# Kernel optimization log

Hardware: AMD Instinct MI355X
Metric: run time of the kernel (lower is better)

The kernel has to match this reference:

```python
import jax, jax.numpy as jnp
import numpy as np
from jax import lax

B, C, W, H = 32, 64, 32, 32
HEADS, RED = 4, 16
D = C // HEADS


def setup_inputs() -> dict:
    key = jax.random.key(0)
    ks = jax.random.split(key, 16)
    s = 0.05
    return {
        "x": jax.random.normal(ks[0], (B, C, W, H), jnp.float32),
        "Wq": jax.random.normal(ks[1], (C, C), jnp.float32) * s,
        "bq": jnp.zeros((C,), jnp.float32),
        "Wk": jax.random.normal(ks[2], (C, C), jnp.float32) * s,
        "bk": jnp.zeros((C,), jnp.float32),
        "Wv": jax.random.normal(ks[3], (C, C), jnp.float32) * s,
        "bv": jnp.zeros((C,), jnp.float32),
        "rel_h": jax.random.normal(ks[4], (1, HEADS, D, 1, H), jnp.float32),
        "rel_w": jax.random.normal(ks[5], (1, HEADS, D, W, 1), jnp.float32),
        "ln_g": jnp.ones((C, W, H), jnp.float32),
        "ln_b": jnp.zeros((C, W, H), jnp.float32),
        "ca_w1": jax.random.normal(ks[6], (C // RED, C), jnp.float32) * s,
        "ca_b1": jnp.zeros((C // RED,), jnp.float32),
        "ca_w2": jax.random.normal(ks[7], (C, C // RED), jnp.float32) * s,
        "ca_b2": jnp.zeros((C,), jnp.float32),
        "sa_w": jax.random.normal(ks[8], (1, 2, 7, 7), jnp.float32) * s,
        "sa_b": jnp.zeros((1,), jnp.float32),
    }


def reference(x, Wq, bq, Wk, bk, Wv, bv, rel_h, rel_w, ln_g, ln_b,
              ca_w1, ca_b1, ca_w2, ca_b2, sa_w, sa_b):
    b, c, w, h = x.shape
    n = w * h
    d = c // HEADS

    def conv1x1(t, wt, bt):
        return jnp.einsum('bchw,oc->bohw', t, wt) + bt[None, :, None, None]

    # ---- MHSA branch ----
    q = conv1x1(x, Wq, bq).reshape(b, HEADS, d, n)
    k = conv1x1(x, Wk, bk).reshape(b, HEADS, d, n)
    v = conv1x1(x, Wv, bv).reshape(b, HEADS, d, n)
    cc = jnp.einsum('bhdi,bhdj->bhij', q, k)                  # content-content
    pos = (rel_h + rel_w).reshape(1, HEADS, d, n)              # [1,H,d,N]
    cp = jnp.einsum('zhdi,bhdj->bhij', pos, q)                 # content-position
    att = jax.nn.softmax(cc + cp, axis=-1)                     # [b,H,N,N]
    out = jnp.einsum('bhdj,bhij->bhdi', v, att).reshape(b, c, w, h)
    # LayerNorm over (C,W,H)
    mu = jnp.mean(out, axis=(1, 2, 3), keepdims=True)
    var = jnp.var(out, axis=(1, 2, 3), keepdims=True)
    ln = (out - mu) * lax.rsqrt(var + 1e-5) * ln_g[None] + ln_b[None]
    mhsa = ln + x

    # ---- CBAM branch ----
    avg = jnp.mean(x, axis=(2, 3))                             # [b,c]
    mx = jnp.max(x, axis=(2, 3))

    def mlp(f):
        hid = jax.nn.relu(jnp.einsum('bc,oc->bo', f, ca_w1) + ca_b1)
        return jnp.einsum('bc,oc->bo', hid, ca_w2) + ca_b2

    ch_att = jax.nn.sigmoid(mlp(avg) + mlp(mx))[:, :, None, None]
    xc = ch_att * x
    feat = jnp.stack([jnp.mean(xc, axis=1), jnp.max(xc, axis=1)], axis=1)  # [b,2,w,h]
    sp = lax.conv_general_dilated(feat, sa_w, (1, 1), 'SAME',
                                  dimension_numbers=('NCHW', 'OIHW', 'NCHW'))
    sp = sp + sa_b[None, :, None, None]
    cbam = jax.nn.sigmoid(sp) * xc

    return mhsa + cbam + x
```

## Files before the change

### kernel.cpp

```cpp
#include <hip/hip_runtime.h>

#define BB 32
#define CC 64
#define WW 32
#define HHT 32
#define NH 4
#define DHD 16
#define NN 1024
#define LOG2E 1.4426950408889634f

typedef __attribute__((ext_vector_type(8))) short bf16x8;
typedef __attribute__((ext_vector_type(4))) float f32x4;

__device__ __forceinline__ float wave_sum(float v) {
#pragma unroll
  for (int off = 32; off > 0; off >>= 1) v += __shfl_down(v, off, 64);
  return v;
}
__device__ __forceinline__ float wave_max(float v) {
#pragma unroll
  for (int off = 32; off > 0; off >>= 1) v = fmaxf(v, __shfl_down(v, off, 64));
  return v;
}
__device__ __forceinline__ unsigned bf16pair(float lo, float hi) {
  unsigned a = __float_as_uint(lo), b = __float_as_uint(hi);
  a += 0x7FFFu + ((a >> 16) & 1u);
  b += 0x7FFFu + ((b >> 16) & 1u);
  return (a >> 16) | (b & 0xFFFF0000u);
}
__device__ __forceinline__ short bf16s(float f) {
  unsigned a = __float_as_uint(f);
  a += 0x7FFFu + ((a >> 16) & 1u);
  return (short)(a >> 16);
}

__global__ __launch_bounds__(256) void qkv_kernel(
    const float* __restrict__ x,
    const float* __restrict__ Wq, const float* __restrict__ bq,
    const float* __restrict__ Wk, const float* __restrict__ bk,
    const float* __restrict__ Wv, const float* __restrict__ bv,
    short* __restrict__ KQ, short* __restrict__ Vb, float* __restrict__ lnzero)
{
  __shared__ __align__(16) short Ws[192 * 72];
  const int tid = threadIdx.x;
  const int b = blockIdx.y, nt = blockIdx.x;

  if (tid < 192) {
    const int m = tid >> 4, dd = tid & 15;
    const int mat = m >> 2, h = m & 3;
    const float* src = (mat == 0 ? Wk : (mat == 1 ? Wq : Wv)) + (h * 16 + dd) * CC;
    const float scale = (mat == 0) ? LOG2E : 1.f;
    short* dst = Ws + tid * 72;
#pragma unroll
    for (int c8 = 0; c8 < 8; ++c8) {
      const float4 f0 = *reinterpret_cast<const float4*>(src + c8 * 8);
      const float4 f1 = *reinterpret_cast<const float4*>(src + c8 * 8 + 4);
      uint4 u;
      u.x = bf16pair(f0.x*scale, f0.y*scale); u.y = bf16pair(f0.z*scale, f0.w*scale);
      u.z = bf16pair(f1.x*scale, f1.y*scale); u.w = bf16pair(f1.z*scale, f1.w*scale);
      *reinterpret_cast<uint4*>(dst + c8 * 8) = u;
    }
  }
  if (blockIdx.x == 0 && blockIdx.y == 0 && tid < 64) lnzero[tid] = 0.f;
  __syncthreads();

  const int wid = tid >> 6, lane = tid & 63, Q = lane >> 4, il = lane & 15;
  const int n = nt * 64 + wid * 16 + il;
  const float* xb = x + (size_t)b * CC * NN;

  union { bf16x8 s; unsigned u[4]; } bfr[2];
#pragma unroll
  for (int half = 0; half < 2; ++half) {
#pragma unroll
    for (int p = 0; p < 4; ++p) {
      const int c0 = 32 * half + 8 * Q + 2 * p;
      const float f0 = xb[(size_t)c0 * NN + n];
      const float f1 = xb[(size_t)(c0 + 1) * NN + n];
      bfr[half].u[p] = bf16pair(f0, f1);
    }
  }

  const f32x4 zero4 = {0.f, 0.f, 0.f, 0.f};
  f32x4 acc[12];
#pragma unroll
  for (int m = 0; m < 12; ++m) {
    const short* wr = Ws + (m * 16 + il) * 72;
    const bf16x8 a0 = *reinterpret_cast<const bf16x8*>(wr + 8 * Q);
    const bf16x8 a1 = *reinterpret_cast<const bf16x8*>(wr + 32 + 8 * Q);
    acc[m] = __builtin_amdgcn_mfma_f32_16x16x32_bf16(a0, bfr[0].s, zero4, 0, 0, 0);
    acc[m] = __builtin_amdgcn_mfma_f32_16x16x32_bf16(a1, bfr[1].s, acc[m], 0, 0, 0);
  }

#pragma unroll
  for (int m = 0; m < 12; ++m) {
    const int mat = m >> 2, h = m & 3;
    const float bsc = (mat == 0) ? LOG2E : 1.f;
    const float4 bias = *reinterpret_cast<const float4*>(
        (mat == 0 ? bk : (mat == 1 ? bq : bv)) + h * 16 + 4 * Q);
    const float v0 = acc[m][0] + bias.x*bsc, v1 = acc[m][1] + bias.y*bsc;
    const float v2 = acc[m][2] + bias.z*bsc, v3 = acc[m][3] + bias.w*bsc;
    if (mat < 2) {
      uint2 pk;
      pk.x = bf16pair(v0, v1); pk.y = bf16pair(v2, v3);
      *reinterpret_cast<uint2*>(KQ + ((size_t)(b * NH + h) * NN + n) * 32 +
                                (mat == 0 ? 0 : 16) + 4 * Q) = pk;
    } else {
      short* vb = Vb + ((size_t)(b * NH + h) * 16 + 4 * Q) * NN + n;
      vb[0]            = bf16s(v0);
      vb[(size_t)NN]   = bf16s(v1);
      vb[2*(size_t)NN] = bf16s(v2);
      vb[3*(size_t)NN] = bf16s(v3);
    }
  }
}

__global__ __launch_bounds__(256) void flash_kernel(
    const short* __restrict__ KQ, const short* __restrict__ Vb,
    const float* __restrict__ rel_h, const float* __restrict__ rel_w,
    float* __restrict__ attnout, float* __restrict__ lnsum, float* __restrict__ lnsum2)
{
  const int tid = threadIdx.x;
  const int wid = tid >> 6, lane = tid & 63;
  const int Q = lane >> 4, il = lane & 15;
  const int bh = blockIdx.x;
  const int h = bh & 3, b = bh >> 2;
  const int ibase = blockIdx.y * 256 + wid * 64;

  bf16x8 bfrag[4];
#pragma unroll
  for (int g2 = 0; g2 < 4; ++g2) {
    const int i = ibase + g2*16 + il;
    if (Q < 2) {
      bfrag[g2] = *reinterpret_cast<const bf16x8*>(KQ + ((size_t)bh*NN + i)*32 + 16 + 8*Q);
    } else {
      const int wrow = i >> 5, hcol = i & 31;
      union { bf16x8 s; unsigned u[4]; } t;
#pragma unroll
      for (int p = 0; p < 4; ++p) {
        const int d0 = 8*(Q-2) + 2*p;
        const float f0 = LOG2E*(rel_h[(h*DHD + d0)*HHT + hcol] + rel_w[(h*DHD + d0)*WW + wrow]);
        const float f1 = LOG2E*(rel_h[(h*DHD + d0+1)*HHT + hcol] + rel_w[(h*DHD + d0+1)*WW + wrow]);
        t.u[p] = bf16pair(f0, f1);
      }
      bfrag[g2] = t.s;
    }
  }

  const short* KQb = KQ + (size_t)bh*NN*32;
  const short* Vbb = Vb + ((size_t)bh*16 + il)*NN;
  const f32x4 zero4 = {0.f, 0.f, 0.f, 0.f};
  f32x4 acc[4] = {zero4, zero4, zero4, zero4};
  float lp[4] = {0.f, 0.f, 0.f, 0.f};

  bf16x8 agc[4]; uint2 vloc[2], vhic[2];
#pragma unroll
  for (int g = 0; g < 4; ++g)
    agc[g] = *reinterpret_cast<const bf16x8*>(KQb + (size_t)(16*g + il)*32 + 8*Q);
#pragma unroll
  for (int hh = 0; hh < 2; ++hh) {
    const short* vp = Vbb + 32*hh + 4*Q;
    vloc[hh] = *reinterpret_cast<const uint2*>(vp);
    vhic[hh] = *reinterpret_cast<const uint2*>(vp + 16);
  }

  for (int jt = 0; jt < NN; jt += 64) {
    const int jn = (jt + 64) & (NN - 1);
    bf16x8 agn[4]; uint2 vlon[2], vhin[2];
#pragma unroll
    for (int g = 0; g < 4; ++g)
      agn[g] = *reinterpret_cast<const bf16x8*>(KQb + (size_t)(jn + 16*g + il)*32 + 8*Q);
#pragma unroll
    for (int hh = 0; hh < 2; ++hh) {
      const short* vp = Vbb + jn + 32*hh + 4*Q;
      vlon[hh] = *reinterpret_cast<const uint2*>(vp);
      vhin[hh] = *reinterpret_cast<const uint2*>(vp + 16);
    }

    union { bf16x8 s; unsigned u[4]; } bv0, bv1;
    bv0.u[0] = vloc[0].x; bv0.u[1] = vloc[0].y; bv0.u[2] = vhic[0].x; bv0.u[3] = vhic[0].y;
    bv1.u[0] = vloc[1].x; bv1.u[1] = vloc[1].y; bv1.u[2] = vhic[1].x; bv1.u[3] = vhic[1].y;

#pragma unroll
    for (int g2 = 0; g2 < 4; ++g2) {
      float p[4][4];
      unsigned pk[4][2];
#pragma unroll
      for (int g = 0; g < 4; ++g) {
        const f32x4 s = __builtin_amdgcn_mfma_f32_16x16x32_bf16(agc[g], bfrag[g2], zero4, 0, 0, 0);
#pragma unroll
        for (int r = 0; r < 4; ++r) { p[g][r] = __builtin_amdgcn_exp2f(s[r]); lp[g2] += p[g][r]; }
        pk[g][0] = bf16pair(p[g][0], p[g][1]);
        pk[g][1] = bf16pair(p[g][2], p[g][3]);
      }
#pragma unroll
      for (int hh = 0; hh < 2; ++hh) {
        union { bf16x8 s; unsigned u[4]; } ap;
        ap.u[0] = pk[2*hh][0];   ap.u[1] = pk[2*hh][1];
        ap.u[2] = pk[2*hh+1][0]; ap.u[3] = pk[2*hh+1][1];
        acc[g2] = __builtin_amdgcn_mfma_f32_16x16x32_bf16(ap.s, hh ? bv1.s : bv0.s, acc[g2], 0, 0, 0);
      }
    }
#pragma unroll
    for (int g = 0; g < 4; ++g) agc[g] = agn[g];
#pragma unroll
    for (int hh = 0; hh < 2; ++hh) { vloc[hh] = vlon[hh]; vhic[hh] = vhin[hh]; }
  }

  float s1 = 0.f, s2 = 0.f;
#pragma unroll
  for (int g2 = 0; g2 < 4; ++g2) {
    float l = lp[g2];
    l += __shfl_xor(l, 16, 64);
    l += __shfl_xor(l, 32, 64);
#pragma unroll
    for (int r = 0; r < 4; ++r) {
      const float li = __shfl(l, 4*Q + r, 64);
      const float v = acc[g2][r] / li;
      const int ig = ibase + g2*16 + 4*Q + r;
      attnout[((size_t)b*CC + h*DHD + il)*NN + ig] = v;
      s1 += v; s2 += v*v;
    }
  }
  s1 = wave_sum(s1); s2 = wave_sum(s2);
  __shared__ float r1[4], r2[4];
  if (lane == 0) { r1[wid] = s1; r2[wid] = s2; }
  __syncthreads();
  if (tid == 0) {
    atomicAdd(&lnsum[b],  r1[0]+r1[1]+r1[2]+r1[3]);
    atomicAdd(&lnsum2[b], r2[0]+r2[1]+r2[2]+r2[3]);
  }
}

__global__ __launch_bounds__(256) void cbamstats_kernel(
    const float* __restrict__ x, float* __restrict__ avg, float* __restrict__ mx)
{
  const int bc = blockIdx.x, tid = threadIdx.x;
  const float* p = x + (size_t)bc*NN;
  float s = 0.f, m = -3.0e38f;
  for (int u = tid; u < NN; u += 256) { const float v = p[u]; s += v; m = fmaxf(m, v); }
  s = wave_sum(s); m = wave_max(m);
  __shared__ float rs[4], rm[4];
  const int wid = tid >> 6, lane = tid & 63;
  if (lane == 0) { rs[wid] = s; rm[wid] = m; }
  __syncthreads();
  if (tid == 0) {
    avg[bc] = (rs[0]+rs[1]+rs[2]+rs[3]) * (1.f/NN);
    mx[bc]  = fmaxf(fmaxf(rm[0], rm[1]), fmaxf(rm[2], rm[3]));
  }
}

__global__ __launch_bounds__(256) void mlpfeat_kernel(
    const float* __restrict__ x, const float* __restrict__ avg, const float* __restrict__ mxv,
    const float* __restrict__ w1, const float* __restrict__ b1,
    const float* __restrict__ w2, const float* __restrict__ b2,
    float* __restrict__ chv, float* __restrict__ feat)
{
  const int b = blockIdx.y, qq = blockIdx.x, tid = threadIdx.x;
  __shared__ float sa[CC], sm[CC], sch[CC];
  __shared__ float ps[4][64], pm[4][64];
  if (tid < CC) { sa[tid] = avg[b*CC + tid]; sm[tid] = mxv[b*CC + tid]; }
  __syncthreads();
  if (tid < CC) {
    float s = 2.f * b2[tid];
#pragma unroll
    for (int o = 0; o < 4; ++o) {
      float ha = b1[o], hm = b1[o];
#pragma unroll
      for (int k = 0; k < CC; ++k) { ha += w1[o*CC + k]*sa[k]; hm += w1[o*CC + k]*sm[k]; }
      s += w2[tid*4 + o] * (fmaxf(ha, 0.f) + fmaxf(hm, 0.f));
    }
    const float c = 1.f/(1.f + __expf(-s));
    sch[tid] = c;
    if (qq == 0) chv[b*CC + tid] = c;
  }
  __syncthreads();
  const int nl = tid & 63, cg = tid >> 6;
  const int n = qq*64 + nl;
  float s = 0.f, m = -3.0e38f;
#pragma unroll
  for (int c = cg*16; c < cg*16 + 16; ++c) {
    const float v = sch[c] * x[((size_t)b*CC + c)*NN + n];
    s += v; m = fmaxf(m, v);
  }
  ps[cg][nl] = s; pm[cg][nl] = m;
  __syncthreads();
  if (cg == 0) {
    const float S = ps[0][nl]+ps[1][nl]+ps[2][nl]+ps[3][nl];
    const float M = fmaxf(fmaxf(pm[0][nl], pm[1][nl]), fmaxf(pm[2][nl], pm[3][nl]));
    feat[(size_t)b*2*NN + n]      = S * (1.f/CC);
    feat[(size_t)b*2*NN + NN + n] = M;
  }
}

__global__ __launch_bounds__(256) void final_kernel(
    const float* __restrict__ x, const float* __restrict__ attn,
    const float* __restrict__ ln_g, const float* __restrict__ ln_b,
    const float* __restrict__ feat, const float* __restrict__ ch,
    const float* __restrict__ lnsum, const float* __restrict__ lnsum2,
    const float* __restrict__ sa_w, const float* __restrict__ sa_b,
    float* __restrict__ out)
{
  const int b = blockIdx.y;
  const int c0 = blockIdx.z * 16;
  const int n = blockIdx.x*256 + threadIdx.x;
  const int w = n >> 5, hh = n & 31;
  __shared__ float sch[CC];
  __shared__ float swt[98];
  if (threadIdx.x < CC) sch[threadIdx.x] = ch[b*CC + threadIdx.x];
  if (threadIdx.x < 98) swt[threadIdx.x] = sa_w[threadIdx.x];
  __syncthreads();

  float s = sa_b[0];
#pragma unroll
  for (int ci = 0; ci < 2; ++ci)
#pragma unroll
    for (int kh = 0; kh < 7; ++kh) {
      const int wy = w + kh - 3;
      if (wy < 0 || wy >= WW) continue;
#pragma unroll
      for (int kw = 0; kw < 7; ++kw) {
        const int hx = hh + kw - 3;
        if (hx < 0 || hx >= HHT) continue;
        s += feat[((size_t)(b*2) + ci)*NN + wy*HHT + hx] * swt[ci*49 + kh*7 + kw];
      }
    }
  const float sg = 1.f/(1.f + __expf(-s));
  const float inv = 1.f/(CC*NN);
  const float m = lnsum[b]*inv;
  const float var = lnsum2[b]*inv - m*m;
  const float r = rsqrtf(var + 1e-5f);
#pragma unroll
  for (int c = c0; c < c0 + 16; ++c) {
    const size_t idx = ((size_t)b*CC + c)*NN + n;
    const float xa = x[idx];
    const float ln = (attn[idx] - m) * r * ln_g[c*NN + n] + ln_b[c*NN + n];
    out[idx] = ln + 2.f*xa + sg * sch[c] * xa;
  }
}

extern "C" void kernel_launch(void* const* d_in, const int* in_sizes, int n_in,
                              void* d_out, int out_size, void* d_ws, size_t ws_size,
                              hipStream_t stream)
{
  const float* x     = (const float*)d_in[0];
  const float* Wq    = (const float*)d_in[1];
  const float* bq    = (const float*)d_in[2];
  const float* Wk    = (const float*)d_in[3];
  const float* bk    = (const float*)d_in[4];
  const float* Wv    = (const float*)d_in[5];
  const float* bv    = (const float*)d_in[6];
  const float* rel_h = (const float*)d_in[7];
  const float* rel_w = (const float*)d_in[8];
  const float* ln_g  = (const float*)d_in[9];
  const float* ln_b  = (const float*)d_in[10];
  const float* cw1   = (const float*)d_in[11];
  const float* cb1   = (const float*)d_in[12];
  const float* cw2   = (const float*)d_in[13];
  const float* cb2   = (const float*)d_in[14];
  const float* saw   = (const float*)d_in[15];
  const float* sab   = (const float*)d_in[16];
  float* out = (float*)d_out;

  short* KQ = (short*)d_ws;
  short* Vb = KQ + (size_t)128*1024*32;
  float* fs = (float*)(Vb + (size_t)128*16*1024);
  float* lnsum  = fs;
  float* lnsum2 = fs + 32;
  float* avg    = fs + 64;
  float* mxv    = avg + 2048;
  float* chv    = mxv + 2048;
  float* feat   = chv + 2048;
  float* attn   = out;

  qkv_kernel<<<dim3(16, BB), 256, 0, stream>>>(x, Wq, bq, Wk, bk, Wv, bv, KQ, Vb, lnsum);
  flash_kernel<<<dim3(BB*NH, 4), 256, 0, stream>>>(KQ, Vb, rel_h, rel_w, attn, lnsum, lnsum2);
  cbamstats_kernel<<<BB*CC, 256, 0, stream>>>(x, avg, mxv);
  mlpfeat_kernel<<<dim3(16, BB), 256, 0, stream>>>(x, avg, mxv, cw1, cb1, cw2, cb2, chv, feat);
  final_kernel<<<dim3(4, BB, 4), 256, 0, stream>>>(x, attn, ln_g, ln_b, feat, chv, lnsum, lnsum2, saw, sab, out);
}
```

Measured before the change: 167.2 us.

## Precompute bf16 weights once, stage KQ stores via LDS, double flash grid

A new one-block prep kernel converts the QKV weights and biases to bf16 (log2e-scaled for K) in global memory once, instead of every qkv block converting them into shared memory. The qkv kernel loops per head and stages K/Q tiles through LDS so that global KQ writes are coalesced. The flash kernel gives each wave 32 query rows instead of 64 and launches twice as many blocks (1024), which raises occupancy and spreads work over more CUs. The cost is that each block streams the full K/V sequence for half as many queries, doubling total K/V reads, and the extra prep launch adds overhead.

```diff
diff --git a/kernel.cpp b/kernel.cpp
--- a/kernel.cpp
+++ b/kernel.cpp
@@ -34,83 +34,94 @@
   return (short)(a >> 16);
 }
 
-__global__ __launch_bounds__(256) void qkv_kernel(
-    const float* __restrict__ x,
+__global__ __launch_bounds__(256) void prep_kernel(
     const float* __restrict__ Wq, const float* __restrict__ bq,
     const float* __restrict__ Wk, const float* __restrict__ bk,
     const float* __restrict__ Wv, const float* __restrict__ bv,
-    short* __restrict__ KQ, short* __restrict__ Vb, float* __restrict__ lnzero)
-{
-  __shared__ __align__(16) short Ws[192 * 72];
+    short* __restrict__ Wb, float* __restrict__ bb, float* __restrict__ lnzero)
+{
   const int tid = threadIdx.x;
-  const int b = blockIdx.y, nt = blockIdx.x;
-
+  for (int idx = tid; idx < 192*32; idx += 256) {
+    const int row = idx >> 5, p = idx & 31;
+    const int m = row >> 4, dd = row & 15, mat = m >> 2, h = m & 3;
+    const float* src = (mat == 0 ? Wk : (mat == 1 ? Wq : Wv)) + (h*16 + dd)*CC + 2*p;
+    const float sc = (mat == 0) ? LOG2E : 1.f;
+    reinterpret_cast<unsigned*>(Wb)[row*32 + p] = bf16pair(src[0]*sc, src[1]*sc);
+  }
   if (tid < 192) {
-    const int m = tid >> 4, dd = tid & 15;
-    const int mat = m >> 2, h = m & 3;
-    const float* src = (mat == 0 ? Wk : (mat == 1 ? Wq : Wv)) + (h * 16 + dd) * CC;
-    const float scale = (mat == 0) ? LOG2E : 1.f;
-    short* dst = Ws + tid * 72;
-#pragma unroll
-    for (int c8 = 0; c8 < 8; ++c8) {
-      const float4 f0 = *reinterpret_cast<const float4*>(src + c8 * 8);
-      const float4 f1 = *reinterpret_cast<const float4*>(src + c8 * 8 + 4);
-      uint4 u;
-      u.x = bf16pair(f0.x*scale, f0.y*scale); u.y = bf16pair(f0.z*scale, f0.w*scale);
-      u.z = bf16pair(f1.x*scale, f1.y*scale); u.w = bf16pair(f1.z*scale, f1.w*scale);
-      *reinterpret_cast<uint4*>(dst + c8 * 8) = u;
-    }
-  }
-  if (blockIdx.x == 0 && blockIdx.y == 0 && tid < 64) lnzero[tid] = 0.f;
-  __syncthreads();
-
+    const int m = tid >> 4, dd = tid & 15, mat = m >> 2, h = m & 3;
+    const float* bs = (mat == 0 ? bk : (mat == 1 ? bq : bv));
+    bb[tid] = bs[h*16 + dd] * ((mat == 0) ? LOG2E : 1.f);
+  }
+  if (tid < 64) lnzero[tid] = 0.f;
+}
+
+__global__ __launch_bounds__(256) void qkv_kernel(
+    const float* __restrict__ x, const short* __restrict__ Wb,
+    const float* __restrict__ bb, short* __restrict__ KQ, short* __restrict__ Vb)
+{
+  __shared__ short KQt[4*16*36];
+  const int tid = threadIdx.x;
   const int wid = tid >> 6, lane = tid & 63, Q = lane >> 4, il = lane & 15;
-  const int n = nt * 64 + wid * 16 + il;
+  const int b = blockIdx.y;
+  const int nbase = blockIdx.x*64 + wid*16;
+  const int n = nbase + il;
   const float* xb = x + (size_t)b * CC * NN;
+  short* tw = KQt + wid*576;
 
   union { bf16x8 s; unsigned u[4]; } bfr[2];
 #pragma unroll
   for (int half = 0; half < 2; ++half) {
 #pragma unroll
     for (int p = 0; p < 4; ++p) {
-      const int c0 = 32 * half + 8 * Q + 2 * p;
-      const float f0 = xb[(size_t)c0 * NN + n];
-      const float f1 = xb[(size_t)(c0 + 1) * NN + n];
+      const int c0 = 32*half + 8*Q + 2*p;
+      const float f0 = xb[(size_t)c0*NN + n];
+      const float f1 = xb[(size_t)(c0+1)*NN + n];
       bfr[half].u[p] = bf16pair(f0, f1);
     }
   }
 
   const f32x4 zero4 = {0.f, 0.f, 0.f, 0.f};
-  f32x4 acc[12];
-#pragma unroll
-  for (int m = 0; m < 12; ++m) {
-    const short* wr = Ws + (m * 16 + il) * 72;
-    const bf16x8 a0 = *reinterpret_cast<const bf16x8*>(wr + 8 * Q);
-    const bf16x8 a1 = *reinterpret_cast<const bf16x8*>(wr + 32 + 8 * Q);
-    acc[m] = __builtin_amdgcn_mfma_f32_16x16x32_bf16(a0, bfr[0].s, zero4, 0, 0, 0);
-    acc[m] = __builtin_amdgcn_mfma_f32_16x16x32_bf16(a1, bfr[1].s, acc[m], 0, 0, 0);
-  }
-
-#pragma unroll
-  for (int m = 0; m < 12; ++m) {
-    const int mat = m >> 2, h = m & 3;
-    const float bsc = (mat == 0) ? LOG2E : 1.f;
-    const float4 bias = *reinterpret_cast<const float4*>(
-        (mat == 0 ? bk : (mat == 1 ? bq : bv)) + h * 16 + 4 * Q);
-    const float v0 = acc[m][0] + bias.x*bsc, v1 = acc[m][1] + bias.y*bsc;
-    const float v2 = acc[m][2] + bias.z*bsc, v3 = acc[m][3] + bias.w*bsc;
-    if (mat < 2) {
-      uint2 pk;
-      pk.x = bf16pair(v0, v1); pk.y = bf16pair(v2, v3);
-      *reinterpret_cast<uint2*>(KQ + ((size_t)(b * NH + h) * NN + n) * 32 +
-                                (mat == 0 ? 0 : 16) + 4 * Q) = pk;
-    } else {
-      short* vb = Vb + ((size_t)(b * NH + h) * 16 + 4 * Q) * NN + n;
-      vb[0]            = bf16s(v0);
-      vb[(size_t)NN]   = bf16s(v1);
-      vb[2*(size_t)NN] = bf16s(v2);
-      vb[3*(size_t)NN] = bf16s(v3);
-    }
+#pragma unroll
+  for (int h = 0; h < NH; ++h) {
+    const short* wk_ = Wb + ((h     )*16 + il)*64;
+    const short* wq_ = Wb + ((4 + h)*16 + il)*64;
+    const short* wv_ = Wb + ((8 + h)*16 + il)*64;
+    f32x4 ak = __builtin_amdgcn_mfma_f32_16x16x32_bf16(
+        *reinterpret_cast<const bf16x8*>(wk_ + 8*Q), bfr[0].s, zero4, 0, 0, 0);
+    ak = __builtin_amdgcn_mfma_f32_16x16x32_bf16(
+        *reinterpret_cast<const bf16x8*>(wk_ + 32 + 8*Q), bfr[1].s, ak, 0, 0, 0);
+    f32x4 aq = __builtin_amdgcn_mfma_f32_16x16x32_bf16(
+        *reinterpret_cast<const bf16x8*>(wq_ + 8*Q), bfr[0].s, zero4, 0, 0, 0);
+    aq = __builtin_amdgcn_mfma_f32_16x16x32_bf16(
+        *reinterpret_cast<const bf16x8*>(wq_ + 32 + 8*Q), bfr[1].s, aq, 0, 0, 0);
+    f32x4 av = __builtin_amdgcn_mfma_f32_16x16x32_bf16(
+        *reinterpret_cast<const bf16x8*>(wv_ + 8*Q), bfr[0].s, zero4, 0, 0, 0);
+    av = __builtin_amdgcn_mfma_f32_16x16x32_bf16(
+        *reinterpret_cast<const bf16x8*>(wv_ + 32 + 8*Q), bfr[1].s, av, 0, 0, 0);
+
+    const float4 bk4 = *reinterpret_cast<const float4*>(bb + (h     )*16 + 4*Q);
+    const float4 bq4 = *reinterpret_cast<const float4*>(bb + (4 + h)*16 + 4*Q);
+    const float4 bv4 = *reinterpret_cast<const float4*>(bb + (8 + h)*16 + 4*Q);
+
+    uint2 ku, qu;
+    ku.x = bf16pair(ak[0]+bk4.x, ak[1]+bk4.y); ku.y = bf16pair(ak[2]+bk4.z, ak[3]+bk4.w);
+    qu.x = bf16pair(aq[0]+bq4.x, aq[1]+bq4.y); qu.y = bf16pair(aq[2]+bq4.z, aq[3]+bq4.w);
+    *reinterpret_cast<uint2*>(&tw[il*36      + 4*Q]) = ku;
+    *reinterpret_cast<uint2*>(&tw[il*36 + 16 + 4*Q]) = qu;
+
+    short* vb = Vb + ((size_t)(b*NH + h)*16 + 4*Q)*NN + n;
+    vb[0]            = bf16s(av[0]+bv4.x);
+    vb[(size_t)NN]   = bf16s(av[1]+bv4.y);
+    vb[2*(size_t)NN] = bf16s(av[2]+bv4.z);
+    vb[3*(size_t)NN] = bf16s(av[3]+bv4.w);
+
+    const int n2 = lane >> 2, cch = lane & 3;
+    const uint2 lo = *reinterpret_cast<const uint2*>(&tw[n2*36      + cch*4]);
+    const uint2 hi = *reinterpret_cast<const uint2*>(&tw[n2*36 + 16 + cch*4]);
+    short* gbase = KQ + ((size_t)(b*NH + h)*NN + nbase + n2)*32;
+    *reinterpret_cast<uint2*>(gbase      + cch*4) = lo;
+    *reinterpret_cast<uint2*>(gbase + 16 + cch*4) = hi;
   }
 }
 
@@ -124,11 +135,11 @@
   const int Q = lane >> 4, il = lane & 15;
   const int bh = blockIdx.x;
   const int h = bh & 3, b = bh >> 2;
-  const int ibase = blockIdx.y * 256 + wid * 64;
-
-  bf16x8 bfrag[4];
-#pragma unroll
-  for (int g2 = 0; g2 < 4; ++g2) {
+  const int ibase = blockIdx.y * 128 + wid * 32;
+
+  bf16x8 bfrag[2];
+#pragma unroll
+  for (int g2 = 0; g2 < 2; ++g2) {
     const int i = ibase + g2*16 + il;
     if (Q < 2) {
       bfrag[g2] = *reinterpret_cast<const bf16x8*>(KQ + ((size_t)bh*NN + i)*32 + 16 + 8*Q);
@@ -149,8 +160,8 @@
   const short* KQb = KQ + (size_t)bh*NN*32;
   const short* Vbb = Vb + ((size_t)bh*16 + il)*NN;
   const f32x4 zero4 = {0.f, 0.f, 0.f, 0.f};
-  f32x4 acc[4] = {zero4, zero4, zero4, zero4};
-  float lp[4] = {0.f, 0.f, 0.f, 0.f};
+  f32x4 acc[2] = {zero4, zero4};
+  float lp[2] = {0.f, 0.f};
 
   bf16x8 agc[4]; uint2 vloc[2], vhic[2];
 #pragma unroll
@@ -181,7 +192,7 @@
     bv1.u[0] = vloc[1].x; bv1.u[1] = vloc[1].y; bv1.u[2] = vhic[1].x; bv1.u[3] = vhic[1].y;
 
 #pragma unroll
-    for (int g2 = 0; g2 < 4; ++g2) {
+    for (int g2 = 0; g2 < 2; ++g2) {
       float p[4][4];
       unsigned pk[4][2];
 #pragma unroll
@@ -208,7 +219,7 @@
 
   float s1 = 0.f, s2 = 0.f;
 #pragma unroll
-  for (int g2 = 0; g2 < 4; ++g2) {
+  for (int g2 = 0; g2 < 2; ++g2) {
     float l = lp[g2];
     l += __shfl_xor(l, 16, 64);
     l += __shfl_xor(l, 32, 64);
@@ -370,10 +381,13 @@
   float* mxv    = avg + 2048;
   float* chv    = mxv + 2048;
   float* feat   = chv + 2048;
+  short* Wb     = (short*)(feat + 65536);
+  float* bb     = (float*)(Wb + 12288);
   float* attn   = out;
 
-  qkv_kernel<<<dim3(16, BB), 256, 0, stream>>>(x, Wq, bq, Wk, bk, Wv, bv, KQ, Vb, lnsum);
-  flash_kernel<<<dim3(BB*NH, 4), 256, 0, stream>>>(KQ, Vb, rel_h, rel_w, attn, lnsum, lnsum2);
+  prep_kernel<<<1, 256, 0, stream>>>(Wq, bq, Wk, bk, Wv, bv, Wb, bb, lnsum);
+  qkv_kernel<<<dim3(16, BB), 256, 0, stream>>>(x, Wb, bb, KQ, Vb);
+  flash_kernel<<<dim3(BB*NH, 8), 256, 0, stream>>>(KQ, Vb, rel_h, rel_w, attn, lnsum, lnsum2);
   cbamstats_kernel<<<BB*CC, 256, 0, stream>>>(x, avg, mxv);
   mlpfeat_kernel<<<dim3(16, BB), 256, 0, stream>>>(x, avg, mxv, cw1, cb1, cw2, cb2, chv, feat);
   final_kernel<<<dim3(4, BB, 4), 256, 0, stream>>>(x, attn, ln_g, ln_b, feat, chv, lnsum, lnsum2, saw, sab, out);
```

Measured after the change: 185.4 us. 1.11x slower.

## Split flash key loop into two interleaved halves and truncate P to bf16

Applied to the files above, without the earlier changes.

The flash attention loop now processes two independent key halves (0-511 and 512-1023) at once, each with its own accumulators and prefetched fragments. The goal is more instruction-level parallelism between the MFMA, exp2 and packing chains. Probabilities are packed to bf16 by truncation with a single perm instruction instead of round-to-nearest, and a launch-bounds occupancy hint is added. The final kernel handles 8 channels per block instead of 16, doubling its grid. This raises register pressure in the flash kernel and slightly changes numerics through truncation.

```diff
diff --git a/kernel.cpp b/kernel.cpp
--- a/kernel.cpp
+++ b/kernel.cpp
@@ -27,6 +27,9 @@
   a += 0x7FFFu + ((a >> 16) & 1u);
   b += 0x7FFFu + ((b >> 16) & 1u);
   return (a >> 16) | (b & 0xFFFF0000u);
+}
+__device__ __forceinline__ unsigned bf16pair_trunc(float lo, float hi) {
+  return __builtin_amdgcn_perm(__float_as_uint(hi), __float_as_uint(lo), 0x07060302u);
 }
 __device__ __forceinline__ short bf16s(float f) {
   unsigned a = __float_as_uint(f);
@@ -114,7 +117,7 @@
   }
 }
 
-__global__ __launch_bounds__(256) void flash_kernel(
+__global__ __launch_bounds__(256, 2) void flash_kernel(
     const short* __restrict__ KQ, const short* __restrict__ Vb,
     const float* __restrict__ rel_h, const float* __restrict__ rel_w,
     float* __restrict__ attnout, float* __restrict__ lnsum, float* __restrict__ lnsum2)
@@ -149,73 +152,113 @@
   const short* KQb = KQ + (size_t)bh*NN*32;
   const short* Vbb = Vb + ((size_t)bh*16 + il)*NN;
   const f32x4 zero4 = {0.f, 0.f, 0.f, 0.f};
-  f32x4 acc[4] = {zero4, zero4, zero4, zero4};
-  float lp[4] = {0.f, 0.f, 0.f, 0.f};
-
-  bf16x8 agc[4]; uint2 vloc[2], vhic[2];
-#pragma unroll
-  for (int g = 0; g < 4; ++g)
-    agc[g] = *reinterpret_cast<const bf16x8*>(KQb + (size_t)(16*g + il)*32 + 8*Q);
+  f32x4 accA[4] = {zero4, zero4, zero4, zero4};
+  f32x4 accB[4] = {zero4, zero4, zero4, zero4};
+  float lpA[4] = {0.f, 0.f, 0.f, 0.f};
+  float lpB[4] = {0.f, 0.f, 0.f, 0.f};
+
+  bf16x8 agA[4], agB[4]; uint2 vloA[2], vhiA[2], vloB[2], vhiB[2];
+#pragma unroll
+  for (int g = 0; g < 4; ++g) {
+    agA[g] = *reinterpret_cast<const bf16x8*>(KQb + (size_t)(      16*g + il)*32 + 8*Q);
+    agB[g] = *reinterpret_cast<const bf16x8*>(KQb + (size_t)(512 + 16*g + il)*32 + 8*Q);
+  }
 #pragma unroll
   for (int hh = 0; hh < 2; ++hh) {
-    const short* vp = Vbb + 32*hh + 4*Q;
-    vloc[hh] = *reinterpret_cast<const uint2*>(vp);
-    vhic[hh] = *reinterpret_cast<const uint2*>(vp + 16);
-  }
-
-  for (int jt = 0; jt < NN; jt += 64) {
-    const int jn = (jt + 64) & (NN - 1);
-    bf16x8 agn[4]; uint2 vlon[2], vhin[2];
-#pragma unroll
-    for (int g = 0; g < 4; ++g)
-      agn[g] = *reinterpret_cast<const bf16x8*>(KQb + (size_t)(jn + 16*g + il)*32 + 8*Q);
+    const short* vpA = Vbb + 32*hh + 4*Q;
+    const short* vpB = Vbb + 512 + 32*hh + 4*Q;
+    vloA[hh] = *reinterpret_cast<const uint2*>(vpA);
+    vhiA[hh] = *reinterpret_cast<const uint2*>(vpA + 16);
+    vloB[hh] = *reinterpret_cast<const uint2*>(vpB);
+    vhiB[hh] = *reinterpret_cast<const uint2*>(vpB + 16);
+  }
+
+  for (int jt = 0; jt < 512; jt += 64) {
+    const int jn = (jt + 64) & 511;
+    bf16x8 agAn[4], agBn[4]; uint2 vloAn[2], vhiAn[2], vloBn[2], vhiBn[2];
+#pragma unroll
+    for (int g = 0; g < 4; ++g) {
+      agAn[g] = *reinterpret_cast<const bf16x8*>(KQb + (size_t)(      jn + 16*g + il)*32 + 8*Q);
+      agBn[g] = *reinterpret_cast<const bf16x8*>(KQb + (size_t)(512 + jn + 16*g + il)*32 + 8*Q);
+    }
 #pragma unroll
     for (int hh = 0; hh < 2; ++hh) {
-      const short* vp = Vbb + jn + 32*hh + 4*Q;
-      vlon[hh] = *reinterpret_cast<const uint2*>(vp);
-      vhin[hh] = *reinterpret_cast<const uint2*>(vp + 16);
-    }
-
-    union { bf16x8 s; unsigned u[4]; } bv0, bv1;
-    bv0.u[0] = vloc[0].x; bv0.u[1] = vloc[0].y; bv0.u[2] = vhic[0].x; bv0.u[3] = vhic[0].y;
-    bv1.u[0] = vloc[1].x; bv1.u[1] = vloc[1].y; bv1.u[2] = vhic[1].x; bv1.u[3] = vhic[1].y;
+      const short* vpA = Vbb + jn + 32*hh + 4*Q;
+      const short* vpB = Vbb + 512 + jn + 32*hh + 4*Q;
+      vloAn[hh] = *reinterpret_cast<const uint2*>(vpA);
+      vhiAn[hh] = *reinterpret_cast<const uint2*>(vpA + 16);
+      vloBn[hh] = *reinterpret_cast<const uint2*>(vpB);
+      vhiBn[hh] = *reinterpret_cast<const uint2*>(vpB + 16);
+    }
+
+    union { bf16x8 s; unsigned u[4]; } bvA0, bvA1, bvB0, bvB1;
+    bvA0.u[0] = vloA[0].x; bvA0.u[1] = vloA[0].y; bvA0.u[2] = vhiA[0].x; bvA0.u[3] = vhiA[0].y;
+    bvA1.u[0] = vloA[1].x; bvA1.u[1] = vloA[1].y; bvA1.u[2] = vhiA[1].x; bvA1.u[3] = vhiA[1].y;
+    bvB0.u[0] = vloB[0].x; bvB0.u[1] = vloB[0].y; bvB0.u[2] = vhiB[0].x; bvB0.u[3] = vhiB[0].y;
+    bvB1.u[0] = vloB[1].x; bvB1.u[1] = vloB[1].y; bvB1.u[2] = vhiB[1].x; bvB1.u[3] = vhiB[1].y;
 
 #pragma unroll
     for (int g2 = 0; g2 < 4; ++g2) {
-      float p[4][4];
-      unsigned pk[4][2];
-#pragma unroll
-      for (int g = 0; g < 4; ++g) {
-        const f32x4 s = __builtin_amdgcn_mfma_f32_16x16x32_bf16(agc[g], bfrag[g2], zero4, 0, 0, 0);
-#pragma unroll
-        for (int r = 0; r < 4; ++r) { p[g][r] = __builtin_amdgcn_exp2f(s[r]); lp[g2] += p[g][r]; }
-        pk[g][0] = bf16pair(p[g][0], p[g][1]);
-        pk[g][1] = bf16pair(p[g][2], p[g][3]);
+      {
+        float p[4][4];
+        unsigned pk[4][2];
+#pragma unroll
+        for (int g = 0; g < 4; ++g) {
+          const f32x4 s = __builtin_amdgcn_mfma_f32_16x16x32_bf16(agA[g], bfrag[g2], zero4, 0, 0, 0);
+#pragma unroll
+          for (int r = 0; r < 4; ++r) p[g][r] = __builtin_amdgcn_exp2f(s[r]);
+          lpA[g2] += (p[g][0] + p[g][1]) + (p[g][2] + p[g][3]);
+          pk[g][0] = bf16pair_trunc(p[g][0], p[g][1]);
+          pk[g][1] = bf16pair_trunc(p[g][2], p[g][3]);
+        }
+#pragma unroll
+        for (int hh = 0; hh < 2; ++hh) {
+          union { bf16x8 s; unsigned u[4]; } ap;
+          ap.u[0] = pk[2*hh][0];   ap.u[1] = pk[2*hh][1];
+          ap.u[2] = pk[2*hh+1][0]; ap.u[3] = pk[2*hh+1][1];
+          accA[g2] = __builtin_amdgcn_mfma_f32_16x16x32_bf16(ap.s, hh ? bvA1.s : bvA0.s, accA[g2], 0, 0, 0);
+        }
       }
-#pragma unroll
-      for (int hh = 0; hh < 2; ++hh) {
-        union { bf16x8 s; unsigned u[4]; } ap;
-        ap.u[0] = pk[2*hh][0];   ap.u[1] = pk[2*hh][1];
-        ap.u[2] = pk[2*hh+1][0]; ap.u[3] = pk[2*hh+1][1];
-        acc[g2] = __builtin_amdgcn_mfma_f32_16x16x32_bf16(ap.s, hh ? bv1.s : bv0.s, acc[g2], 0, 0, 0);
+      {
+        float p[4][4];
+        unsigned pk[4][2];
+#pragma unroll
+        for (int g = 0; g < 4; ++g) {
+          const f32x4 s = __builtin_amdgcn_mfma_f32_16x16x32_bf16(agB[g], bfrag[g2], zero4, 0, 0, 0);
+#pragma unroll
+          for (int r = 0; r < 4; ++r) p[g][r] = __builtin_amdgcn_exp2f(s[r]);
+          lpB[g2] += (p[g][0] + p[g][1]) + (p[g][2] + p[g][3]);
+          pk[g][0] = bf16pair_trunc(p[g][0], p[g][1]);
+          pk[g][1] = bf16pair_trunc(p[g][2], p[g][3]);
+        }
+#pragma unroll
+        for (int hh = 0; hh < 2; ++hh) {
+          union { bf16x8 s; unsigned u[4]; } ap;
+          ap.u[0] = pk[2*hh][0];   ap.u[1] = pk[2*hh][1];
+          ap.u[2] = pk[2*hh+1][0]; ap.u[3] = pk[2*hh+1][1];
+          accB[g2] = __builtin_amdgcn_mfma_f32_16x16x32_bf16(ap.s, hh ? bvB1.s : bvB0.s, accB[g2], 0, 0, 0);
+        }
       }
     }
 #pragma unroll
-    for (int g = 0; g < 4; ++g) agc[g] = agn[g];
-#pragma unroll
-    for (int hh = 0; hh < 2; ++hh) { vloc[hh] = vlon[hh]; vhic[hh] = vhin[hh]; }
+    for (int g = 0; g < 4; ++g) { agA[g] = agAn[g]; agB[g] = agBn[g]; }
+#pragma unroll
+    for (int hh = 0; hh < 2; ++hh) {
+      vloA[hh] = vloAn[hh]; vhiA[hh] = vhiAn[hh];
+      vloB[hh] = vloBn[hh]; vhiB[hh] = vhiBn[hh];
+    }
   }
 
   float s1 = 0.f, s2 = 0.f;
 #pragma unroll
   for (int g2 = 0; g2 < 4; ++g2) {
-    float l = lp[g2];
+    float l = lpA[g2] + lpB[g2];
     l += __shfl_xor(l, 16, 64);
     l += __shfl_xor(l, 32, 64);
 #pragma unroll
     for (int r = 0; r < 4; ++r) {
       const float li = __shfl(l, 4*Q + r, 64);
-      const float v = acc[g2][r] / li;
+      const float v = (accA[g2][r] + accB[g2][r]) / li;
       const int ig = ibase + g2*16 + 4*Q + r;
       attnout[((size_t)b*CC + h*DHD + il)*NN + ig] = v;
       s1 += v; s2 += v*v;
@@ -301,7 +344,7 @@
     float* __restrict__ out)
 {
   const int b = blockIdx.y;
-  const int c0 = blockIdx.z * 16;
+  const int c0 = blockIdx.z * 8;
   const int n = blockIdx.x*256 + threadIdx.x;
   const int w = n >> 5, hh = n & 31;
   __shared__ float sch[CC];
@@ -330,7 +373,7 @@
   const float var = lnsum2[b]*inv - m*m;
   const float r = rsqrtf(var + 1e-5f);
 #pragma unroll
-  for (int c = c0; c < c0 + 16; ++c) {
+  for (int c = c0; c < c0 + 8; ++c) {
     const size_t idx = ((size_t)b*CC + c)*NN + n;
     const float xa = x[idx];
     const float ln = (attn[idx] - m) * r * ln_g[c*NN + n] + ln_b[c*NN + n];
@@ -376,5 +419,5 @@
   flash_kernel<<<dim3(BB*NH, 4), 256, 0, stream>>>(KQ, Vb, rel_h, rel_w, attn, lnsum, lnsum2);
   cbamstats_kernel<<<BB*CC, 256, 0, stream>>>(x, avg, mxv);
   mlpfeat_kernel<<<dim3(16, BB), 256, 0, stream>>>(x, avg, mxv, cw1, cb1, cw2, cb2, chv, feat);
-  final_kernel<<<dim3(4, BB, 4), 256, 0, stream>>>(x, attn, ln_g, ln_b, feat, chv, lnsum, lnsum2, saw, sab, out);
-}
+  final_kernel<<<dim3(4, BB, 8), 256, 0, stream>>>(x, attn, ln_g, ln_b, feat, chv, lnsum, lnsum2, saw, sab, out);
+}
```

Measured after the change: 175.2 us. +4.8%, slower.
